# Kernel optimization log

Hardware: AMD Instinct MI355X
Metric: run time of the kernel (lower is better)

The kernel has to match this reference:

```python
import jax, jax.numpy as jnp
import numpy as np

CH = 512
NUM_HEADS = 8
NUM_GROUPS = 32  # min(32, channels)
EPS = 1e-5


def setup_inputs() -> dict:
    key = jax.random.key(0)
    ks = jax.random.split(key, 4)
    B, C, H, W = 8, CH, 32, 32
    x = jax.random.normal(ks[0], (B, C, H, W), dtype=jnp.float32)
    gn_weight = jnp.ones((C,), dtype=jnp.float32)
    gn_bias = jnp.zeros((C,), dtype=jnp.float32)
    # 1x1 conv weights stored as [out_ch, in_ch] (kernel dims squeezed)
    qkv_weight = jax.random.normal(ks[1], (3 * C, C), dtype=jnp.float32) * (C ** -0.5)
    qkv_bias = jnp.zeros((3 * C,), dtype=jnp.float32)
    proj_weight = jax.random.normal(ks[2], (C, C), dtype=jnp.float32) * (C ** -0.5)
    proj_bias = jnp.zeros((C,), dtype=jnp.float32)
    return {
        "x": x,
        "gn_weight": gn_weight,
        "gn_bias": gn_bias,
        "qkv_weight": qkv_weight,
        "qkv_bias": qkv_bias,
        "proj_weight": proj_weight,
        "proj_bias": proj_bias,
    }


def _group_norm(x, weight, bias):
    B, C, H, W = x.shape
    g = x.reshape(B, NUM_GROUPS, C // NUM_GROUPS, H, W)
    mean = jnp.mean(g, axis=(2, 3, 4), keepdims=True)
    var = jnp.var(g, axis=(2, 3, 4), keepdims=True)
    g = (g - mean) * jax.lax.rsqrt(var + EPS)
    g = g.reshape(B, C, H, W)
    return g * weight[None, :, None, None] + bias[None, :, None, None]


def reference(x, gn_weight, gn_bias, qkv_weight, qkv_bias, proj_weight, proj_bias):
    B, C, H, W = x.shape
    nh = NUM_HEADS
    hc = C // nh
    N = H * W

    h = _group_norm(x, gn_weight, gn_bias)
    # 1x1 conv == per-pixel matmul
    qkv = jnp.einsum('oc,bchw->bohw', qkv_weight, h) + qkv_bias[None, :, None, None]
    q, k, v = jnp.split(qkv, 3, axis=1)
    # b (h c) x y -> b h c (x y)
    q = q.reshape(B, nh, hc, N)
    k = k.reshape(B, nh, hc, N)
    v = v.reshape(B, nh, hc, N)

    scale = hc ** -0.5
    attn = jnp.einsum('bhci,bhcj->bhij', q, k) * scale  # [B, nh, N, N]
    attn = jax.nn.softmax(attn, axis=-1)
    out = jnp.einsum('bhij,bhcj->bhci', attn, v)  # [B, nh, hc, N]
    out = out.reshape(B, C, H, W)
    out = jnp.einsum('oc,bchw->bohw', proj_weight, out) + proj_bias[None, :, None, None]
    return x + out
```

## Files before the change

kernel.cpp:

```cpp
#include <hip/hip_runtime.h>
#include <math.h>

#define B_   8
#define C_   512
#define N_   1024
#define NH_  8
#define HC_  64

typedef __attribute__((ext_vector_type(8))) short bf16x8;
typedef __attribute__((ext_vector_type(4))) float f32x4;
typedef __attribute__((ext_vector_type(16))) float f32x16;

#define MFMA16(a, b, c) __builtin_amdgcn_mfma_f32_16x16x32_bf16(a, b, c, 0, 0, 0)
#define MFMA32(a, b, c) __builtin_amdgcn_mfma_f32_32x32x16_bf16(a, b, c, 0, 0, 0)

__device__ __forceinline__ unsigned short f2bf(float f) {
  unsigned u = __builtin_bit_cast(unsigned, f);
  u += 0x7fffu + ((u >> 16) & 1u);
  return (unsigned short)(u >> 16);
}

__device__ __forceinline__ unsigned short f2bf_trunc(float f) {
  return (unsigned short)(__builtin_bit_cast(unsigned, f) >> 16);
}

__device__ __forceinline__ unsigned pack2(float a, float b) {
  return (unsigned)f2bf(a) | ((unsigned)f2bf(b) << 16);
}

__device__ __forceinline__ void gll16(const void* g, void* l) {
  __builtin_amdgcn_global_load_lds(
      (const __attribute__((address_space(1))) unsigned int*)g,
      (__attribute__((address_space(3))) unsigned int*)l, 16, 0, 0);
}

__global__ __launch_bounds__(256) void prep(const float* __restrict__ x,
                                            const float* __restrict__ gw,
                                            const float* __restrict__ gb,
                                            const float* __restrict__ qkvw,
                                            const float* __restrict__ pw,
                                            unsigned short* __restrict__ hT,
                                            unsigned short* __restrict__ qkvw_bf,
                                            unsigned short* __restrict__ projw_bf) {
  const int t = threadIdx.x;
  if (blockIdx.x >= 256) {
    const int widx = blockIdx.x - 256;
    const float* src = (widx < 768) ? qkvw : pw;
    unsigned short* dst = (widx < 768) ? qkvw_bf : projw_bf;
    const int i = ((widx < 768) ? widx : widx - 768) * 1024 + t * 4;
    const float4 v = *(const float4*)(src + i);
    ushort4 o;
    o.x = f2bf(v.x); o.y = f2bf(v.y); o.z = f2bf(v.z); o.w = f2bf(v.w);
    *(ushort4*)(dst + i) = o;
    return;
  }
  const int b = blockIdx.x >> 5;
  const int g = blockIdx.x & 31;
  const float* xg = x + ((size_t)b * C_ + (size_t)g * 16) * N_;

  float4 xv[16];
  float s = 0.f, ss = 0.f;
#pragma unroll
  for (int k = 0; k < 16; ++k) {
    xv[k] = *(const float4*)(xg + (size_t)k * N_ + t * 4);
    s  += xv[k].x + xv[k].y + xv[k].z + xv[k].w;
    ss += xv[k].x * xv[k].x + xv[k].y * xv[k].y + xv[k].z * xv[k].z + xv[k].w * xv[k].w;
  }
#pragma unroll
  for (int off = 32; off > 0; off >>= 1) {
    s  += __shfl_down(s, off);
    ss += __shfl_down(ss, off);
  }
  __shared__ float rs[4], rss[4], sh_mi[2];
  if ((t & 63) == 0) { rs[t >> 6] = s; rss[t >> 6] = ss; }
  __syncthreads();
  if (t == 0) {
    s  = rs[0] + rs[1] + rs[2] + rs[3];
    ss = rss[0] + rss[1] + rss[2] + rss[3];
    const float mean = s * (1.f / 16384.f);
    const float var  = ss * (1.f / 16384.f) - mean * mean;
    sh_mi[0] = mean;
    sh_mi[1] = rsqrtf(var + 1e-5f);
  }
  __syncthreads();
  const float mean = sh_mi[0], inv = sh_mi[1];

  float sc[16], of[16];
#pragma unroll
  for (int k = 0; k < 16; ++k) {
    const int c = g * 16 + k;
    sc[k] = inv * gw[c];
    of[k] = gb[c] - mean * sc[k];
  }
#pragma unroll
  for (int r = 0; r < 4; ++r) {
    const int p = t * 4 + r;
    unsigned short* dst = hT + ((size_t)b * N_ + p) * C_ + g * 16;
    uint4 o0, o1;
#pragma unroll
    for (int k2 = 0; k2 < 4; ++k2) {
      const float a0 = ((const float*)&xv[k2 * 2 + 0])[r] * sc[k2 * 2 + 0] + of[k2 * 2 + 0];
      const float a1 = ((const float*)&xv[k2 * 2 + 1])[r] * sc[k2 * 2 + 1] + of[k2 * 2 + 1];
      ((unsigned*)&o0)[k2] = pack2(a0, a1);
      const float b0 = ((const float*)&xv[8 + k2 * 2 + 0])[r] * sc[8 + k2 * 2 + 0] + of[8 + k2 * 2 + 0];
      const float b1 = ((const float*)&xv[8 + k2 * 2 + 1])[r] * sc[8 + k2 * 2 + 1] + of[8 + k2 * 2 + 1];
      ((unsigned*)&o1)[k2] = pack2(b0, b1);
    }
    *(uint4*)(dst)     = o0;
    *(uint4*)(dst + 8) = o1;
  }
}

__global__ __launch_bounds__(256, 3) void gemm_qkv(
    const unsigned short* __restrict__ A, const float* __restrict__ bias,
    const unsigned short* __restrict__ BT, unsigned short* __restrict__ qkTout,
    unsigned short* __restrict__ vout) {
  __shared__ __attribute__((aligned(16))) short lds[128 * 136];
  const int t = threadIdx.x;
  const int lane = t & 63, w = t >> 6;
  const int lm = lane & 15, q = lane >> 4;
  const int wm = w >> 1, wn = w & 1;
  const int b = blockIdx.z;
  const int m0 = blockIdx.y * 128, n0 = blockIdx.x * 128;
  const unsigned short* Bb = BT + (size_t)b * N_ * C_;

  f32x4 acc[4][4];
#pragma unroll
  for (int i = 0; i < 4; ++i)
#pragma unroll
    for (int j = 0; j < 4; ++j) acc[i][j] = (f32x4){0.f, 0.f, 0.f, 0.f};

#define QKV_STAGE(k0, base_)                                                   \
  {                                                                            \
    _Pragma("unroll") for (int rr = 0; rr < 2; ++rr) {                         \
      const int rg = w * 2 + rr;                                               \
      gll16(A  + (size_t)(m0 + rg * 16 + lm) * C_ + (k0) + q * 8,              \
            (base_) + rg * 512);                                               \
      gll16(Bb + (size_t)(n0 + rg * 16 + lm) * C_ + (k0) + q * 8,              \
            (base_) + (8 + rg) * 512);                                         \
    }                                                                          \
  }

#define QKV_COMPUTE(base_)                                                     \
  {                                                                            \
    bf16x8 af[4];                                                              \
    _Pragma("unroll") for (int mi = 0; mi < 4; ++mi)                           \
      af[mi] = *(const bf16x8*)((base_) + (wm * 4 + mi) * 512 + lane * 8);     \
    _Pragma("unroll") for (int ni = 0; ni < 4; ++ni) {                         \
      const bf16x8 bfr =                                                       \
          *(const bf16x8*)((base_) + (8 + wn * 4 + ni) * 512 + lane * 8);      \
      _Pragma("unroll") for (int mi = 0; mi < 4; ++mi)                         \
        acc[mi][ni] = MFMA16(af[mi], bfr, acc[mi][ni]);                        \
    }                                                                          \
  }

  QKV_STAGE(0, lds)
  for (int it = 0; it < 15; ++it) {
    __syncthreads();
    short* nxt = lds + ((it + 1) & 1) * 8192;
    QKV_STAGE((it + 1) * 32, nxt)
    const short* cur = lds + (it & 1) * 8192;
    QKV_COMPUTE(cur)
  }
  __syncthreads();
  QKV_COMPUTE(lds + 8192)
#undef QKV_STAGE
#undef QKV_COMPUTE

  __syncthreads();
  if (blockIdx.y < 8) {
    const float qs = (blockIdx.y < 4) ? 0.18033688011112042f : 1.0f;
#pragma unroll
    for (int mi = 0; mi < 4; ++mi) {
#pragma unroll
      for (int ni = 0; ni < 4; ++ni) {
        const int pl = wn * 64 + ni * 16 + lm;
        const int ol0 = wm * 64 + mi * 16 + q * 4;
        ushort4 o4;
        o4.x = f2bf((acc[mi][ni][0] + bias[m0 + ol0 + 0]) * qs);
        o4.y = f2bf((acc[mi][ni][1] + bias[m0 + ol0 + 1]) * qs);
        o4.z = f2bf((acc[mi][ni][2] + bias[m0 + ol0 + 2]) * qs);
        o4.w = f2bf((acc[mi][ni][3] + bias[m0 + ol0 + 3]) * qs);
        *(ushort4*)&lds[pl * 136 + ol0] = o4;
      }
    }
    __syncthreads();
#pragma unroll
    for (int u = 0; u < 8; ++u) {
      const int flat = u * 256 + t;
      const int oc = flat & 15, pl = flat >> 4;
      *(uint4*)&qkTout[((size_t)b * N_ + n0 + pl) * 1024 + m0 + oc * 8] =
          *(const uint4*)&lds[pl * 136 + oc * 8];
    }
  } else {
#pragma unroll
    for (int mi = 0; mi < 4; ++mi)
#pragma unroll
      for (int ni = 0; ni < 4; ++ni) {
        const int pl = wn * 64 + ni * 16 + lm;
#pragma unroll
        for (int r = 0; r < 4; ++r) {
          const int ol = wm * 64 + mi * 16 + q * 4 + r;
          lds[ol * 136 + pl] = f2bf(acc[mi][ni][r] + bias[m0 + ol]);
        }
      }
    __syncthreads();
    const int c0 = m0 - 1024;
#pragma unroll
    for (int u = 0; u < 8; ++u) {
      const int flat = u * 256 + t;
      const int pc = flat & 15, ol = flat >> 4;
      *(uint4*)&vout[((size_t)b * 512 + c0 + ol) * N_ + n0 + pc * 8] =
          *(const uint4*)&lds[ol * 136 + pc * 8];
    }
  }
}

__global__ __launch_bounds__(256, 4) void gemm_proj(
    const unsigned short* __restrict__ A, const float* __restrict__ bias,
    const unsigned short* __restrict__ BT, const float* __restrict__ resid,
    float* __restrict__ outf) {
  __shared__ __attribute__((aligned(16))) short lds[32 * 512];
  const int t = threadIdx.x;
  const int lane = t & 63, w = t >> 6;
  const int lm = lane & 15, q = lane >> 4;
  const int wm = w >> 1, wn = w & 1;
  const int b = blockIdx.z;
  const int m0 = blockIdx.y * 64, n0 = blockIdx.x * 64;
  const unsigned short* Bb = BT + (size_t)b * N_ * C_;

  f32x4 acc[2][2];
#pragma unroll
  for (int i = 0; i < 2; ++i)
#pragma unroll
    for (int j = 0; j < 2; ++j) acc[i][j] = (f32x4){0.f, 0.f, 0.f, 0.f};

  for (int k0 = 0; k0 < C_; k0 += 128) {
    __syncthreads();
#pragma unroll
    for (int ks = 0; ks < 4; ++ks) {
      gll16(A  + (size_t)(m0 + w * 16 + lm) * C_ + k0 + ks * 32 + q * 8,
            lds + (w * 4 + ks) * 512);
      gll16(Bb + (size_t)(n0 + w * 16 + lm) * C_ + k0 + ks * 32 + q * 8,
            lds + (16 + w * 4 + ks) * 512);
    }
    __syncthreads();
#pragma unroll
    for (int ks = 0; ks < 4; ++ks) {
      bf16x8 af[2];
#pragma unroll
      for (int mi = 0; mi < 2; ++mi)
        af[mi] = *(const bf16x8*)(lds + ((wm * 2 + mi) * 4 + ks) * 512 + lane * 8);
#pragma unroll
      for (int ni = 0; ni < 2; ++ni) {
        const bf16x8 bfr =
            *(const bf16x8*)(lds + (16 + (wn * 2 + ni) * 4 + ks) * 512 + lane * 8);
#pragma unroll
        for (int mi = 0; mi < 2; ++mi)
          acc[mi][ni] = MFMA16(af[mi], bfr, acc[mi][ni]);
      }
    }
  }

#pragma unroll
  for (int mi = 0; mi < 2; ++mi)
#pragma unroll
    for (int ni = 0; ni < 2; ++ni) {
      const int col = n0 + wn * 32 + ni * 16 + lm;
#pragma unroll
      for (int r = 0; r < 4; ++r) {
        const int row = m0 + wm * 32 + mi * 16 + q * 4 + r;
        const size_t oi = ((size_t)b * 512 + row) * N_ + col;
        outf[oi] = acc[mi][ni][r] + bias[row] + resid[oi];
      }
    }
}

__global__ __launch_bounds__(256, 2) void attn_mfma(
    const unsigned short* __restrict__ qkT, const unsigned short* __restrict__ vbuf,
    unsigned short* __restrict__ aoT) {
  __shared__ __attribute__((aligned(16))) short lds[21504];
  short* Ks = lds;
  short* Vs = lds + 8192;
  short* Pb = lds + 12288;

  const int t = threadIdx.x;
  const int l = t & 63, w = t >> 6;
  const int l31 = l & 31, lh = l >> 5;
  const int id = blockIdx.x;
  const int xcd = id & 7, slot = id >> 3;
  const int pair = xcd * 8 + (slot >> 3);
  const int b = pair >> 3, hh = pair & 7;
  const int i0 = (slot & 7) * 128;

  const unsigned short* QT = qkT + (size_t)b * N_ * 1024;
  const unsigned short* Vp = vbuf + ((size_t)b * 512 + hh * 64) * N_;
  short* Pw = Pb + w * 2304;
  char* Pwb = (char*)Pw;

  bf16x8 af[4];
#pragma unroll
  for (int kc = 0; kc < 4; ++kc)
    af[kc] = *(const bf16x8*)(QT + (size_t)(i0 + w * 32 + l31) * 1024 +
                              hh * 64 + kc * 16 + lh * 8);

  bf16x8 ones;
#pragma unroll
  for (int e = 0; e < 8; ++e) ones[e] = (short)0x3F80;

  f32x16 accO[2], accL;
#pragma unroll
  for (int r2 = 0; r2 < 16; ++r2) {
    accL[r2] = 0.f; accO[0][r2] = 0.f; accO[1][r2] = 0.f;
  }

#pragma unroll
  for (int rr = 0; rr < 2; ++rr) {
    const int idx = w * 2 + rr, jb = idx >> 2, kc = idx & 3;
    gll16(QT + (size_t)(jb * 32 + l31) * 1024 + 512 + hh * 64 + kc * 16 + lh * 8,
          Ks + idx * 512);
  }

  const int e2 = (l & 7) << 1;
  const int keyb = ((l31 >> 3) & 1) << 6;
  const int wbase0 = (((l31 >> 3) & 1) << 9) + (lh << 6) + e2;
  const int prd = ((l >> 3) & 7) << 4;

  for (int jt = 0; jt < 16; ++jt) {
    const int j0 = jt * 64;
    __syncthreads();
#pragma unroll
    for (int rr = 0; rr < 2; ++rr) {
      const int idx = w * 2 + rr, nc = idx >> 2, kj = idx & 3;
      gll16(Vp + (size_t)(nc * 32 + l31) * N_ + j0 + kj * 16 + lh * 8,
            Vs + idx * 512);
    }
    if (jt < 15) {
#pragma unroll
      for (int rr = 0; rr < 2; ++rr) {
        const int idx = w * 2 + rr, jb = idx >> 2, kc = idx & 3;
        gll16(QT + (size_t)(j0 + 64 + jb * 32 + l31) * 1024 + 512 + hh * 64 +
                  kc * 16 + lh * 8,
              Ks + ((jt + 1) & 1) * 4096 + idx * 512);
      }
    }
    const short* Kc = Ks + (jt & 1) * 4096;

    f32x16 accS[2];
#pragma unroll
    for (int r2 = 0; r2 < 16; ++r2) { accS[0][r2] = 0.f; accS[1][r2] = 0.f; }
    __builtin_amdgcn_s_setprio(1);
#pragma unroll
    for (int kc = 0; kc < 4; ++kc)
#pragma unroll
      for (int jb = 0; jb < 2; ++jb) {
        const bf16x8 bfr = *(const bf16x8*)(Kc + (jb * 4 + kc) * 512 + l * 8);
        accS[jb] = MFMA32(af[kc], bfr, accS[jb]);
      }
    __builtin_amdgcn_s_setprio(0);

#pragma unroll
    for (int jb = 0; jb < 2; ++jb) {
      const int base = ((jb * 2 + (l31 >> 4)) << 10) + wbase0;
#pragma unroll
      for (int rg = 0; rg < 16; ++rg) {
        const float p = __builtin_exp2f(accS[jb][rg]);
        const int byte = (base + ((rg & 3) << 4) + ((rg >> 2) << 7)) ^
                         ((((rg >> 2) << 4)) | keyb);
        *(short*)(Pwb + byte) = (short)f2bf_trunc(p);
      }
    }

    __syncthreads();

    __builtin_amdgcn_s_setprio(1);
    bf16x8 pa[4];
#pragma unroll
    for (int kj = 0; kj < 4; ++kj)
      pa[kj] = *(const bf16x8*)(Pwb + ((kj << 10) + ((l * 16) ^ prd)));
#pragma unroll
    for (int nc = 0; nc < 2; ++nc)
#pragma unroll
      for (int kj = 0; kj < 4; ++kj) {
        const bf16x8 vf = *(const bf16x8*)(Vs + (nc * 4 + kj) * 512 + l * 8);
        accO[nc] = MFMA32(pa[kj], vf, accO[nc]);
      }
#pragma unroll
    for (int kj = 0; kj < 4; ++kj) accL = MFMA32(pa[kj], ones, accL);
    __builtin_amdgcn_s_setprio(0);
  }

  float linv[16];
#pragma unroll
  for (int rg = 0; rg < 16; ++rg) linv[rg] = 1.f / accL[rg];
#pragma unroll
  for (int nc = 0; nc < 2; ++nc)
#pragma unroll
    for (int rg = 0; rg < 16; ++rg) {
      const int rowi = (rg & 3) + ((rg >> 2) << 3) + (lh << 2);
      Pw[rowi * 72 + nc * 32 + l31] = (short)f2bf(accO[nc][rg] * linv[rg]);
    }
  unsigned short* aob = aoT + (size_t)b * N_ * C_;
#pragma unroll
  for (int u = 0; u < 4; ++u) {
    const int flat = u * 64 + l;
    const int c8 = flat & 7, row = flat >> 3;
    *(uint4*)&aob[(size_t)(i0 + w * 32 + row) * C_ + hh * 64 + c8 * 8] =
        *(const uint4*)&Pw[row * 72 + c8 * 8];
  }
}

extern "C" void kernel_launch(void* const* d_in, const int* in_sizes, int n_in,
                              void* d_out, int out_size, void* d_ws, size_t ws_size,
                              hipStream_t stream) {
  const float* x    = (const float*)d_in[0];
  const float* gw   = (const float*)d_in[1];
  const float* gb   = (const float*)d_in[2];
  const float* qkvw = (const float*)d_in[3];
  const float* qkvb = (const float*)d_in[4];
  const float* pw   = (const float*)d_in[5];
  const float* pb   = (const float*)d_in[6];
  float* out = (float*)d_out;

  unsigned short* hT       = (unsigned short*)d_ws;
  unsigned short* qkvw_bf  = hT + (size_t)B_ * N_ * C_;
  unsigned short* projw_bf = qkvw_bf + 1536 * 512;
  unsigned short* qkT      = projw_bf + 512 * 512;
  unsigned short* vbuf     = qkT + (size_t)B_ * N_ * 1024;
  unsigned short* aoTp     = vbuf + (size_t)B_ * 512 * N_;

  prep<<<1280, 256, 0, stream>>>(x, gw, gb, qkvw, pw, hT, qkvw_bf, projw_bf);
  gemm_qkv<<<dim3(8, 12, B_), 256, 0, stream>>>(qkvw_bf, qkvb, hT, qkT, vbuf);
  attn_mfma<<<512, 256, 0, stream>>>(qkT, vbuf, aoTp);
  gemm_proj<<<dim3(16, 8, B_), 256, 0, stream>>>(projw_bf, pb, aoTp, x, out);
}
```

Before: 162.3 us.

## Keep softmax probabilities in registers via transposed QK^T and permlane swaps

```diff
diff --git a/kernel.cpp b/kernel.cpp
--- a/kernel.cpp
+++ b/kernel.cpp
@@ -296,7 +296,6 @@
   const unsigned short* QT = qkT + (size_t)b * N_ * 1024;
   const unsigned short* Vp = vbuf + ((size_t)b * 512 + hh * 64) * N_;
   short* Pw = Pb + w * 2304;
-  char* Pwb = (char*)Pw;
 
   bf16x8 af[4];
 #pragma unroll
@@ -304,15 +303,10 @@
     af[kc] = *(const bf16x8*)(QT + (size_t)(i0 + w * 32 + l31) * 1024 +
                               hh * 64 + kc * 16 + lh * 8);
 
-  bf16x8 ones;
-#pragma unroll
-  for (int e = 0; e < 8; ++e) ones[e] = (short)0x3F80;
-
-  f32x16 accO[2], accL;
-#pragma unroll
-  for (int r2 = 0; r2 < 16; ++r2) {
-    accL[r2] = 0.f; accO[0][r2] = 0.f; accO[1][r2] = 0.f;
-  }
+  f32x16 accO[2];
+#pragma unroll
+  for (int r2 = 0; r2 < 16; ++r2) { accO[0][r2] = 0.f; accO[1][r2] = 0.f; }
+  float lrun = 0.f;
 
 #pragma unroll
   for (int rr = 0; rr < 2; ++rr) {
@@ -320,11 +314,6 @@
     gll16(QT + (size_t)(jb * 32 + l31) * 1024 + 512 + hh * 64 + kc * 16 + lh * 8,
           Ks + idx * 512);
   }
-
-  const int e2 = (l & 7) << 1;
-  const int keyb = ((l31 >> 3) & 1) << 6;
-  const int wbase0 = (((l31 >> 3) & 1) << 9) + (lh << 6) + e2;
-  const int prd = ((l >> 3) & 7) << 4;
 
   for (int jt = 0; jt < 16; ++jt) {
     const int j0 = jt * 64;
@@ -354,51 +343,64 @@
     for (int kc = 0; kc < 4; ++kc)
 #pragma unroll
       for (int jb = 0; jb < 2; ++jb) {
-        const bf16x8 bfr = *(const bf16x8*)(Kc + (jb * 4 + kc) * 512 + l * 8);
-        accS[jb] = MFMA32(af[kc], bfr, accS[jb]);
+        const bf16x8 kfr = *(const bf16x8*)(Kc + (jb * 4 + kc) * 512 + l * 8);
+        accS[jb] = MFMA32(kfr, af[kc], accS[jb]);
       }
     __builtin_amdgcn_s_setprio(0);
 
+    uint4 pa4[4];
 #pragma unroll
     for (int jb = 0; jb < 2; ++jb) {
-      const int base = ((jb * 2 + (l31 >> 4)) << 10) + wbase0;
+      float p[16];
 #pragma unroll
       for (int rg = 0; rg < 16; ++rg) {
-        const float p = __builtin_exp2f(accS[jb][rg]);
-        const int byte = (base + ((rg & 3) << 4) + ((rg >> 2) << 7)) ^
-                         ((((rg >> 2) << 4)) | keyb);
-        *(short*)(Pwb + byte) = (short)f2bf_trunc(p);
+        p[rg] = __builtin_exp2f(accS[jb][rg]);
+        lrun += p[rg];
+      }
+      unsigned own[8];
+#pragma unroll
+      for (int i2 = 0; i2 < 8; ++i2)
+        asm("v_cvt_pk_bf16_f32 %0, %1, %2"
+            : "=v"(own[i2]) : "v"(p[2 * i2]), "v"(p[2 * i2 + 1]));
+#pragma unroll
+      for (int m = 0; m < 2; ++m) {
+        unsigned x0 = own[4 * m + 0], y0 = own[4 * m + 2];
+        unsigned x1 = own[4 * m + 1], y1 = own[4 * m + 3];
+        asm("v_permlane32_swap_b32 %0, %1" : "+v"(x0), "+v"(y0));
+        asm("v_permlane32_swap_b32 %0, %1" : "+v"(x1), "+v"(y1));
+        pa4[jb * 2 + m] = (uint4){x0, x1, y0, y1};
       }
     }
 
     __syncthreads();
 
     __builtin_amdgcn_s_setprio(1);
-    bf16x8 pa[4];
-#pragma unroll
-    for (int kj = 0; kj < 4; ++kj)
-      pa[kj] = *(const bf16x8*)(Pwb + ((kj << 10) + ((l * 16) ^ prd)));
-#pragma unroll
-    for (int nc = 0; nc < 2; ++nc)
-#pragma unroll
-      for (int kj = 0; kj < 4; ++kj) {
+#pragma unroll
+    for (int kj = 0; kj < 4; ++kj) {
+      const bf16x8 pf = __builtin_bit_cast(bf16x8, pa4[kj]);
+#pragma unroll
+      for (int nc = 0; nc < 2; ++nc) {
         const bf16x8 vf = *(const bf16x8*)(Vs + (nc * 4 + kj) * 512 + l * 8);
-        accO[nc] = MFMA32(pa[kj], vf, accO[nc]);
-      }
-#pragma unroll
-    for (int kj = 0; kj < 4; ++kj) accL = MFMA32(pa[kj], ones, accL);
+        accO[nc] = MFMA32(pf, vf, accO[nc]);
+      }
+    }
     __builtin_amdgcn_s_setprio(0);
   }
 
-  float linv[16];
-#pragma unroll
-  for (int rg = 0; rg < 16; ++rg) linv[rg] = 1.f / accL[rg];
+  const float lr = lrun + __shfl_xor(lrun, 32);
+  float* lw = (float*)Pw;
+  lw[l31] = 1.f / lr;
+  float linvr[16];
+#pragma unroll
+  for (int rg = 0; rg < 16; ++rg)
+    linvr[rg] = lw[(rg & 3) + ((rg >> 2) << 3) + (lh << 2)];
+
 #pragma unroll
   for (int nc = 0; nc < 2; ++nc)
 #pragma unroll
     for (int rg = 0; rg < 16; ++rg) {
       const int rowi = (rg & 3) + ((rg >> 2) << 3) + (lh << 2);
-      Pw[rowi * 72 + nc * 32 + l31] = (short)f2bf(accO[nc][rg] * linv[rg]);
+      Pw[rowi * 72 + nc * 32 + l31] = (short)f2bf(accO[nc][rg] * linvr[rg]);
     }
   unsigned short* aob = aoT + (size_t)b * N_ * C_;
 #pragma unroll
```

New measurement: 163.8 us. No clear change (+0.9%).
